# Performance work log

Hardware: AMD Instinct MI355X
Metric: run time of the kernel (lower is better)

The kernel has to match this reference:

```python
import jax, jax.numpy as jnp
import numpy as np

EPS = 1e-12  # torch F.normalize default eps
NUM_HEADS = 8


def _l2norm(t):
    # normalize along last (spatial) axis, matching F.normalize(dim=-1)
    n = jnp.linalg.norm(t, axis=-1, keepdims=True)
    return t / jnp.maximum(n, EPS)


def setup_inputs() -> dict:
    key = jax.random.key(0)
    ks = jax.random.split(key, 5)
    b, dim, qc, h, w = 16, 384, 192, 64, 64
    x = jax.random.normal(ks[0], (b, dim, h, w), dtype=jnp.float32)
    query = jax.random.normal(ks[1], (b, qc, h, w), dtype=jnp.float32)
    w_kv = jax.random.normal(ks[2], (2 * dim, dim), dtype=jnp.float32) * 0.05
    w_q = jax.random.normal(ks[3], (dim, qc), dtype=jnp.float32) * 0.05
    w_proj = jax.random.normal(ks[4], (dim, dim), dtype=jnp.float32) * 0.05
    temperature = jnp.ones((NUM_HEADS, 1, 1), dtype=jnp.float32)
    return {"x": x, "query": query, "w_kv": w_kv, "w_q": w_q,
            "w_proj": w_proj, "temperature": temperature}


def reference(x, query, w_kv, w_q, w_proj, temperature):
    b, c, h, w = x.shape
    hd = NUM_HEADS
    dc = c // hd  # per-head channel dim
    # 1x1 convs == channel GEMMs
    kv = jnp.einsum('oc,bchw->bohw', w_kv, x)          # [b, 2c, h, w]
    k, v = jnp.split(kv, 2, axis=1)                     # each [b, c, h, w]
    q = jnp.einsum('oc,bchw->bohw', w_q, query)         # [b, c, h, w]
    # split heads, flatten spatial: b (head c) h w -> b head c (h w)
    def heads(t):
        return t.reshape(b, hd, dc, h * w)
    q, k, v = heads(q), heads(k), heads(v)
    q = _l2norm(q)
    k = _l2norm(k)
    # channel-wise attention: [b, head, dc, dc]
    attn = jnp.einsum('bhcn,bhdn->bhcd', q, k) * temperature
    attn = jax.nn.softmax(attn, axis=-1)
    out = jnp.einsum('bhcd,bhdn->bhcn', attn, v)        # [b, head, dc, hw]
    out = out.reshape(b, c, h, w)
    out = jnp.einsum('oc,bchw->bohw', w_proj, out)
    return out
```

## Files before the change

kernel.cpp:

```cpp
#include <hip/hip_runtime.h>
#include <hip/hip_bf16.h>

typedef float f4 __attribute__((ext_vector_type(4)));
typedef short s8 __attribute__((ext_vector_type(8)));
typedef short s4 __attribute__((ext_vector_type(4)));

__device__ __forceinline__ short f2bf(float f) {
  union { float f; unsigned u; } v; v.f = f;
  unsigned r = v.u + 0x7fffu + ((v.u >> 16) & 1u);
  return (short)(r >> 16);
}
__device__ __forceinline__ void gl16(const short* g, short* l) {
  __builtin_amdgcn_global_load_lds(
      (const __attribute__((address_space(1))) unsigned*)g,
      (__attribute__((address_space(3))) unsigned*)l, 16, 0, 0);
}

__global__ __launch_bounds__(256, 1)
void kqs_k(const short* __restrict__ xT, const short* __restrict__ qT,
           const short* __restrict__ wkb, const short* __restrict__ wqb,
           float* __restrict__ Spart, float* __restrict__ ssq,
           float* __restrict__ ssk) {
  __shared__ __align__(16) short Bq[64 * 192];
  __shared__ __align__(16) short Bx[64 * 384];
  __shared__ __align__(16) short Qt[192 * 64];
  __shared__ __align__(16) short Kt[192 * 64];
  const int orig = blockIdx.x;
  const int xcd = orig & 7, ix = orig >> 3;
  const int pair = xcd * 16 + (ix >> 1);
  const int hg = ix & 1;
  const int b = pair >> 3, sc = pair & 7;
  const int tid = threadIdx.x, lane = tid & 63, w = tid >> 6;
  const int l15 = lane & 15, lhi = lane >> 4;

  const short* qTb = qT + ((long)b * 4096 + sc * 512) * 192;
  const short* xTb = xT + ((long)b * 4096 + sc * 512) * 384;

  f4 Sacc[3][3];
#pragma unroll
  for (int i = 0; i < 3; ++i)
#pragma unroll
    for (int j = 0; j < 3; ++j) Sacc[i][j] = (f4){0.f, 0.f, 0.f, 0.f};
  float sqa[12], ska[12];
#pragma unroll
  for (int i = 0; i < 12; ++i) { sqa[i] = 0.f; ska[i] = 0.f; }

#pragma unroll
  for (int i = 0; i < 6; ++i) {
    const int q = i * 256 + tid, row = q / 24, c = q % 24;
    gl16(qTb + row * 192 + ((c ^ (row & 7)) * 8), &Bq[q * 8]);
  }
#pragma unroll
  for (int i = 0; i < 12; ++i) {
    const int q = i * 256 + tid, row = q / 48, c = q % 48;
    gl16(xTb + row * 384 + ((c ^ (row & 7)) * 8), &Bx[q * 8]);
  }

#pragma unroll 1
  for (int t = 0; t < 8; ++t) {
    asm volatile("s_waitcnt vmcnt(12)" ::: "memory");
    __builtin_amdgcn_s_barrier();
    __builtin_amdgcn_sched_barrier(0);

    {
      f4 acc[3][4];
#pragma unroll
      for (int i = 0; i < 3; ++i)
#pragma unroll
        for (int j = 0; j < 4; ++j) acc[i][j] = (f4){0.f, 0.f, 0.f, 0.f};
#pragma unroll 2
      for (int kk = 0; kk < 192; kk += 32) {
        s8 af[3], bf[4];
#pragma unroll
        for (int mi = 0; mi < 3; ++mi)
          af[mi] = *(const s8*)(wqb +
              (long)(hg * 192 + w * 48 + mi * 16 + l15) * 192 + kk + lhi * 8);
#pragma unroll
        for (int ni = 0; ni < 4; ++ni) {
          const int s_ = ni * 16 + l15;
          bf[ni] = *(const s8*)(&Bq[s_ * 192 +
                                    ((((kk >> 3) + lhi) ^ (s_ & 7)) << 3)]);
        }
#pragma unroll
        for (int mi = 0; mi < 3; ++mi)
#pragma unroll
          for (int ni = 0; ni < 4; ++ni)
            acc[mi][ni] = __builtin_amdgcn_mfma_f32_16x16x32_bf16(
                af[mi], bf[ni], acc[mi][ni], 0, 0, 0);
      }
#pragma unroll
      for (int mi = 0; mi < 3; ++mi)
#pragma unroll
        for (int r = 0; r < 4; ++r) {
          const int row = w * 48 + mi * 16 + lhi * 4 + r;
#pragma unroll
          for (int ni = 0; ni < 4; ++ni) {
            const int col = ni * 16 + l15;
            const float v = acc[mi][ni][r];
            Qt[row * 64 + (((col >> 3) ^ (row & 7)) << 3) + (col & 7)] =
                f2bf(v);
            sqa[mi * 4 + r] += v * v;
          }
        }
    }

    asm volatile("s_waitcnt vmcnt(0)" ::: "memory");
    __builtin_amdgcn_s_barrier();
    __builtin_amdgcn_sched_barrier(0);

    {
      f4 acc[3][4];
#pragma unroll
      for (int i = 0; i < 3; ++i)
#pragma unroll
        for (int j = 0; j < 4; ++j) acc[i][j] = (f4){0.f, 0.f, 0.f, 0.f};
#pragma unroll 2
      for (int kk = 0; kk < 384; kk += 32) {
        s8 af[3], bf[4];
#pragma unroll
        for (int mi = 0; mi < 3; ++mi)
          af[mi] = *(const s8*)(wkb +
              (long)(hg * 192 + w * 48 + mi * 16 + l15) * 384 + kk + lhi * 8);
#pragma unroll
        for (int ni = 0; ni < 4; ++ni) {
          const int s_ = ni * 16 + l15;
          bf[ni] = *(const s8*)(&Bx[s_ * 384 +
                                    ((((kk >> 3) + lhi) ^ (s_ & 7)) << 3)]);
        }
#pragma unroll
        for (int mi = 0; mi < 3; ++mi)
#pragma unroll
          for (int ni = 0; ni < 4; ++ni)
            acc[mi][ni] = __builtin_amdgcn_mfma_f32_16x16x32_bf16(
                af[mi], bf[ni], acc[mi][ni], 0, 0, 0);
      }
#pragma unroll
      for (int mi = 0; mi < 3; ++mi)
#pragma unroll
        for (int r = 0; r < 4; ++r) {
          const int row = w * 48 + mi * 16 + lhi * 4 + r;
#pragma unroll
          for (int ni = 0; ni < 4; ++ni) {
            const int col = ni * 16 + l15;
            const float v = acc[mi][ni][r];
            Kt[row * 64 + (((col >> 3) ^ (row & 7)) << 3) + (col & 7)] =
                f2bf(v);
            ska[mi * 4 + r] += v * v;
          }
        }
    }

    __builtin_amdgcn_s_barrier();

    if (t + 1 < 8) {
      const long so = (long)(t + 1) * 64;
#pragma unroll
      for (int i = 0; i < 6; ++i) {
        const int q = i * 256 + tid, row = q / 24, c = q % 24;
        gl16(qTb + (so + row) * 192 + ((c ^ (row & 7)) * 8), &Bq[q * 8]);
      }
#pragma unroll
      for (int i = 0; i < 12; ++i) {
        const int q = i * 256 + tid, row = q / 48, c = q % 48;
        gl16(xTb + (so + row) * 384 + ((c ^ (row & 7)) * 8), &Bx[q * 8]);
      }
    }

    {
      const int hl = w * 48;
#pragma unroll
      for (int kk = 0; kk < 64; kk += 32) {
        s8 qa[3], ka[3];
#pragma unroll
        for (int i = 0; i < 3; ++i) {
          const int rr = hl + i * 16 + l15;
          const int cb = (((kk >> 3) + lhi) ^ (rr & 7)) << 3;
          qa[i] = *(const s8*)(&Qt[rr * 64 + cb]);
          ka[i] = *(const s8*)(&Kt[rr * 64 + cb]);
        }
#pragma unroll
        for (int mi = 0; mi < 3; ++mi)
#pragma unroll
          for (int ni = 0; ni < 3; ++ni)
            Sacc[mi][ni] = __builtin_amdgcn_mfma_f32_16x16x32_bf16(
                qa[mi], ka[ni], Sacc[mi][ni], 0, 0, 0);
      }
    }
  }

#pragma unroll
  for (int mi = 0; mi < 3; ++mi)
#pragma unroll
    for (int r = 0; r < 4; ++r) {
      float tq = sqa[mi * 4 + r], tk = ska[mi * 4 + r];
      tq += __shfl_xor(tq, 1); tq += __shfl_xor(tq, 2);
      tq += __shfl_xor(tq, 4); tq += __shfl_xor(tq, 8);
      tk += __shfl_xor(tk, 1); tk += __shfl_xor(tk, 2);
      tk += __shfl_xor(tk, 4); tk += __shfl_xor(tk, 8);
      const int row = hg * 192 + w * 48 + mi * 16 + lhi * 4 + r;
      if (l15 == 0) {
        atomicAdd(&ssq[b * 384 + row], tq);
        atomicAdd(&ssk[b * 384 + row], tk);
      }
    }
  float* Sp = Spart + (((long)sc * 16 + b) * 8 + hg * 4 + w) * 2304;
#pragma unroll
  for (int mi = 0; mi < 3; ++mi)
#pragma unroll
    for (int ni = 0; ni < 3; ++ni)
#pragma unroll
      for (int r = 0; r < 4; ++r)
        Sp[(mi * 16 + lhi * 4 + r) * 48 + ni * 16 + l15] = Sacc[mi][ni][r];
}

template<int NKT, bool OUTF32, bool SWZ>
__global__ __launch_bounds__(256)
void gemm4(const short* __restrict__ A_, long Asb, int lda,
           const short* __restrict__ B_, long Bsb, int ldb,
           void* __restrict__ O_, long Osb, int ldo,
           int nbm, int nbn) {
  __shared__ __align__(16) short As[2][8192];
  __shared__ __align__(16) short Bs[2][8192];
  int f = blockIdx.x;
  if (SWZ) { const int cpx = gridDim.x >> 3; f = (f & 7) * cpx + (f >> 3); }
  const int m0 = (f % nbm) * 128;
  const int t2 = f / nbm;
  const int n0 = (t2 % nbn) * 128;
  const int bz = t2 / nbn;
  const short* Ag = A_ + (long)bz * Asb;
  const short* Bg = B_ + (long)bz * Bsb;

  const int tid = threadIdx.x, lane = tid & 63, wid = tid >> 6;
  const int l15 = lane & 15, lhi = lane >> 4;
  const int wm = (wid >> 1) * 64, wn = (wid & 1) * 64;
  const int srow = tid >> 3;
  const int skc = ((tid & 7) ^ (srow & 7)) * 8;

  f4 acc[4][4];
#pragma unroll
  for (int i = 0; i < 4; ++i)
#pragma unroll
    for (int j = 0; j < 4; ++j) acc[i][j] = (f4){0.f, 0.f, 0.f, 0.f};

#pragma unroll
  for (int it = 0; it < 4; ++it) {
    const int r = it * 32 + srow;
    gl16(Ag + (long)(m0 + r) * lda + skc, &As[0][(it * 256 + tid) * 8]);
    gl16(Bg + (long)(n0 + r) * ldb + skc, &Bs[0][(it * 256 + tid) * 8]);
  }
  if (NKT > 1) {
#pragma unroll
    for (int it = 0; it < 4; ++it) {
      const int r = it * 32 + srow;
      gl16(Ag + (long)(m0 + r) * lda + 64 + skc, &As[1][(it * 256 + tid) * 8]);
      gl16(Bg + (long)(n0 + r) * ldb + 64 + skc, &Bs[1][(it * 256 + tid) * 8]);
    }
  }

#pragma unroll
  for (int kt = 0; kt < NKT; ++kt) {
    const int cur = kt & 1;
    if (kt + 1 < NKT) asm volatile("s_waitcnt vmcnt(8)" ::: "memory");
    else              asm volatile("s_waitcnt vmcnt(0)" ::: "memory");
    __builtin_amdgcn_s_barrier();
    __builtin_amdgcn_sched_barrier(0);
#pragma unroll
    for (int kk = 0; kk < 2; ++kk) {
      const int cb = ((lhi + kk * 4) ^ (l15 & 7)) * 8;
      s8 af[4], bf[4];
#pragma unroll
      for (int i = 0; i < 4; ++i) {
        af[i] = *(const s8*)(&As[cur][(wm + i * 16 + l15) * 64 + cb]);
        bf[i] = *(const s8*)(&Bs[cur][(wn + i * 16 + l15) * 64 + cb]);
      }
#pragma unroll
      for (int mi = 0; mi < 4; ++mi)
#pragma unroll
        for (int ni = 0; ni < 4; ++ni)
          acc[mi][ni] = __builtin_amdgcn_mfma_f32_16x16x32_bf16(
              af[mi], bf[ni], acc[mi][ni], 0, 0, 0);
    }
    asm volatile("s_waitcnt lgkmcnt(0)" ::: "memory");
    __builtin_amdgcn_s_barrier();
    if (kt + 2 < NKT) {
      const int k2 = (kt + 2) * 64;
#pragma unroll
      for (int it = 0; it < 4; ++it) {
        const int r = it * 32 + srow;
        gl16(Ag + (long)(m0 + r) * lda + k2 + skc,
             &As[cur][(it * 256 + tid) * 8]);
        gl16(Bg + (long)(n0 + r) * ldb + k2 + skc,
             &Bs[cur][(it * 256 + tid) * 8]);
      }
    }
  }

#pragma unroll
  for (int mi = 0; mi < 4; ++mi)
#pragma unroll
    for (int r = 0; r < 4; ++r) {
      const int grow = m0 + wm + mi * 16 + lhi * 4 + r;
#pragma unroll
      for (int ni = 0; ni < 4; ++ni) {
        const int col = n0 + wn + ni * 16 + l15;
        const float v = acc[mi][ni][r];
        if (OUTF32)
          ((float*)O_)[(long)bz * Osb + (long)grow * ldo + col] = v;
        else
          ((short*)O_)[(long)bz * Osb + (long)grow * ldo + col] = f2bf(v);
      }
    }
}

__global__ __launch_bounds__(256)
void prep_k(const float* __restrict__ x, const float* __restrict__ q,
            const float* __restrict__ wkv, const float* __restrict__ wq,
            const float* __restrict__ wp, short* __restrict__ xT,
            short* __restrict__ qT, short* __restrict__ wkb,
            short* __restrict__ wvT, short* __restrict__ wqb,
            short* __restrict__ wpb, float* __restrict__ ssqk) {
  const int role = blockIdx.x;
  if (role == 9) {
    const int g = (blockIdx.z * 64 + blockIdx.y) * 256 + threadIdx.x;
    if (g < 12288) ssqk[g] = 0.f;
    for (int i = g; i < 516096; i += 262144) {
      if (i < 147456) {
        wkb[i] = f2bf(wkv[i]);
      } else if (i < 294912) {
        const int t = i - 147456;
        wvT[t] = f2bf(wkv[(384 + (t % 384)) * 384 + t / 384]);
      } else if (i < 368640) {
        wqb[i - 294912] = f2bf(wq[i - 294912]);
      } else {
        wpb[i - 368640] = f2bf(wp[i - 368640]);
      }
    }
    return;
  }
  __shared__ float Ls[64][65];
  const bool isQ = role >= 6;
  const int C = isQ ? 192 : 384;
  const int c0 = (isQ ? role - 6 : role) * 64;
  const int s0 = blockIdx.y * 64;
  const float* src = (isQ ? q : x) + (long)blockIdx.z * C * 4096;
  short* dst = (isQ ? qT : xT) + (long)blockIdx.z * 4096 * C;
  const int tid = threadIdx.x;
  const int rr = tid >> 4, cq = (tid & 15) * 4;
#pragma unroll
  for (int it = 0; it < 4; ++it) {
    const int r = it * 16 + rr;
    f4 v = *(const f4*)(src + (long)(c0 + r) * 4096 + s0 + cq);
    Ls[r][cq + 0] = v.x; Ls[r][cq + 1] = v.y;
    Ls[r][cq + 2] = v.z; Ls[r][cq + 3] = v.w;
  }
  __syncthreads();
#pragma unroll
  for (int it = 0; it < 4; ++it) {
    const int sr = it * 16 + rr;
    s4 o;
#pragma unroll
    for (int j = 0; j < 4; ++j) o[j] = f2bf(Ls[cq + j][sr]);
    *(s4*)(&dst[(long)(s0 + sr) * C + c0 + cq]) = o;
  }
}

__global__ __launch_bounds__(256)
void smY_k(const float* __restrict__ Spart, const float* __restrict__ ssq,
           const float* __restrict__ ssk, const float* __restrict__ temp,
           const short* __restrict__ wpb, short* __restrict__ Yb) {
  const int b = blockIdx.x, h = blockIdx.y, tid = threadIdx.x;
  __shared__ float L[2304];
  __shared__ float rq[48], rk[48], mrow[48], irow[48];
  __shared__ __align__(16) short PTl[48 * 72];
  if (tid < 48) {
    rq[tid] = 1.f / fmaxf(sqrtf(ssq[b * 384 + h * 48 + tid]), 1e-12f);
    rk[tid] = 1.f / fmaxf(sqrtf(ssk[b * 384 + h * 48 + tid]), 1e-12f);
  }
  __syncthreads();
  const float tp = temp[h];
  for (int i = tid; i < 2304; i += 256) {
    float v = 0.f;
#pragma unroll
    for (int z = 0; z < 8; ++z)
      v += Spart[(((long)z * 16 + b) * 8 + h) * 2304 + i];
    const int c = i / 48, d = i % 48;
    L[i] = v * rq[c] * rk[d] * tp;
  }
  __syncthreads();
  if (tid < 48) {
    float m = -1e30f;
    for (int d = 0; d < 48; ++d) m = fmaxf(m, L[tid * 48 + d]);
    float s = 0.f;
    for (int d = 0; d < 48; ++d) s += __expf(L[tid * 48 + d] - m);
    mrow[tid] = m;
    irow[tid] = 1.f / s;
  }
  __syncthreads();
  for (int i = tid; i < 48 * 72; i += 256) {
    const int d = i / 72, c = i % 72;
    float p = 0.f;
    if (c < 48) p = __expf(L[c * 48 + d] - mrow[c]) * irow[c];
    PTl[i] = f2bf(p);
  }
  __syncthreads();
  const int lane = tid & 63, w = tid >> 6;
  const int l15 = lane & 15, lhi = lane >> 4;
  f4 acc[6][3];
#pragma unroll
  for (int i = 0; i < 6; ++i)
#pragma unroll
    for (int j = 0; j < 3; ++j) acc[i][j] = (f4){0.f, 0.f, 0.f, 0.f};
#pragma unroll
  for (int kk = 0; kk < 2; ++kk) {
    s8 bf[3];
#pragma unroll
    for (int ni = 0; ni < 3; ++ni)
      bf[ni] = *(const s8*)(&PTl[(ni * 16 + l15) * 72 + kk * 32 + lhi * 8]);
#pragma unroll
    for (int mi = 0; mi < 6; ++mi) {
      const int row = w * 96 + mi * 16 + l15;
      s8 af = *(const s8*)(wpb + (long)row * 384 + h * 48 + kk * 32 + lhi * 8);
#pragma unroll
      for (int ni = 0; ni < 3; ++ni)
        acc[mi][ni] = __builtin_amdgcn_mfma_f32_16x16x32_bf16(
            af, bf[ni], acc[mi][ni], 0, 0, 0);
    }
  }
#pragma unroll
  for (int mi = 0; mi < 6; ++mi)
#pragma unroll
    for (int r = 0; r < 4; ++r) {
      const int row = w * 96 + mi * 16 + lhi * 4 + r;
#pragma unroll
      for (int ni = 0; ni < 3; ++ni) {
        const int d = ni * 16 + l15;
        Yb[((long)b * 384 + row) * 384 + h * 48 + d] = f2bf(acc[mi][ni][r]);
      }
    }
}

extern "C" void kernel_launch(void* const* d_in, const int* in_sizes, int n_in,
                              void* d_out, int out_size, void* d_ws, size_t ws_size,
                              hipStream_t stream) {
  const float* x = (const float*)d_in[0];
  const float* query = (const float*)d_in[1];
  const float* w_kv = (const float*)d_in[2];
  const float* w_q = (const float*)d_in[3];
  const float* w_proj = (const float*)d_in[4];
  const float* temp = (const float*)d_in[5];

  char* w = (char*)d_ws;
  short* xT   = (short*)(w + 0);
  short* qT   = (short*)(w + 50331648);
  float* Spart= (float*)(w + 75497472);
  short* Yb   = (short*)(w + 94371840);
  short* Nbb  = (short*)(w + 99090432);
  float* ssq  = (float*)(w + 103809024);
  float* ssk  = (float*)(w + 103833600);
  short* wkb  = (short*)(w + 103858176);
  short* wvT  = (short*)(w + 104153088);
  short* wqb  = (short*)(w + 104448000);
  short* wpb  = (short*)(w + 104595456);
  float* out  = (float*)d_out;

  prep_k<<<dim3(10, 64, 16), 256, 0, stream>>>(
      x, query, w_kv, w_q, w_proj, xT, qT, wkb, wvT, wqb, wpb, ssq);
  kqs_k<<<256, 256, 0, stream>>>(xT, qT, wkb, wqb, Spart, ssq, ssk);
  smY_k<<<dim3(16, 8), 256, 0, stream>>>(Spart, ssq, ssk, temp, wpb, Yb);
  gemm4<6, false, false><<<144, 256, 0, stream>>>(
      Yb, 147456, 384, wvT, 0, 384, Nbb, 147456, 384, 3, 3);
  gemm4<6, true, true><<<1536, 256, 0, stream>>>(
      Nbb, 147456, 384, xT, 1572864, 384, out, 1572864, 4096, 3, 32);
}
```

Before: 189.3 us.

## Drop LDS staging in kqs_k, read B fragments from global, double grid

The kernel no longer stages x/query tiles in shared memory through async global-to-LDS loads with barriers. Each wave now reads its MFMA B fragments straight from global memory, and the per-wave Qt/Kt rows are private to that wave, so all block barriers are removed. The spatial split doubles to 16 chunks (512 blocks, launch bounds allowing 2 blocks per CU) and the softmax kernel sums 16 partial S tiles. The goal is more parallelism and occupancy. The cost is that the four waves load the same activation tile redundantly, relying on the caches, and the reduction has more partials.

```diff
diff --git a/kernel.cpp b/kernel.cpp
--- a/kernel.cpp
+++ b/kernel.cpp
@@ -16,25 +16,26 @@
       (__attribute__((address_space(3))) unsigned*)l, 16, 0, 0);
 }
 
-__global__ __launch_bounds__(256, 1)
+__global__ __launch_bounds__(256, 2)
 void kqs_k(const short* __restrict__ xT, const short* __restrict__ qT,
            const short* __restrict__ wkb, const short* __restrict__ wqb,
            float* __restrict__ Spart, float* __restrict__ ssq,
            float* __restrict__ ssk) {
-  __shared__ __align__(16) short Bq[64 * 192];
-  __shared__ __align__(16) short Bx[64 * 384];
   __shared__ __align__(16) short Qt[192 * 64];
   __shared__ __align__(16) short Kt[192 * 64];
   const int orig = blockIdx.x;
   const int xcd = orig & 7, ix = orig >> 3;
-  const int pair = xcd * 16 + (ix >> 1);
+  const int pair = xcd * 32 + (ix >> 1);
   const int hg = ix & 1;
-  const int b = pair >> 3, sc = pair & 7;
+  const int b = pair >> 4, sc = pair & 15;
   const int tid = threadIdx.x, lane = tid & 63, w = tid >> 6;
   const int l15 = lane & 15, lhi = lane >> 4;
-
-  const short* qTb = qT + ((long)b * 4096 + sc * 512) * 192;
-  const short* xTb = xT + ((long)b * 4096 + sc * 512) * 384;
+  const int hl = w * 48;
+
+  const short* qTb = qT + (long)b * 4096 * 192;
+  const short* xTb = xT + (long)b * 4096 * 384;
+  const short* wqw = wqb + (long)(hg * 192 + hl) * 192;
+  const short* wkw = wkb + (long)(hg * 192 + hl) * 384;
 
   f4 Sacc[3][3];
 #pragma unroll
@@ -45,22 +46,9 @@
 #pragma unroll
   for (int i = 0; i < 12; ++i) { sqa[i] = 0.f; ska[i] = 0.f; }
 
-#pragma unroll
-  for (int i = 0; i < 6; ++i) {
-    const int q = i * 256 + tid, row = q / 24, c = q % 24;
-    gl16(qTb + row * 192 + ((c ^ (row & 7)) * 8), &Bq[q * 8]);
-  }
-#pragma unroll
-  for (int i = 0; i < 12; ++i) {
-    const int q = i * 256 + tid, row = q / 48, c = q % 48;
-    gl16(xTb + row * 384 + ((c ^ (row & 7)) * 8), &Bx[q * 8]);
-  }
-
 #pragma unroll 1
-  for (int t = 0; t < 8; ++t) {
-    asm volatile("s_waitcnt vmcnt(12)" ::: "memory");
-    __builtin_amdgcn_s_barrier();
-    __builtin_amdgcn_sched_barrier(0);
+  for (int t = 0; t < 4; ++t) {
+    const int s0 = sc * 256 + t * 64;
 
     {
       f4 acc[3][4];
@@ -68,19 +56,16 @@
       for (int i = 0; i < 3; ++i)
 #pragma unroll
         for (int j = 0; j < 4; ++j) acc[i][j] = (f4){0.f, 0.f, 0.f, 0.f};
-#pragma unroll 2
+#pragma unroll
       for (int kk = 0; kk < 192; kk += 32) {
         s8 af[3], bf[4];
 #pragma unroll
         for (int mi = 0; mi < 3; ++mi)
-          af[mi] = *(const s8*)(wqb +
-              (long)(hg * 192 + w * 48 + mi * 16 + l15) * 192 + kk + lhi * 8);
-#pragma unroll
-        for (int ni = 0; ni < 4; ++ni) {
-          const int s_ = ni * 16 + l15;
-          bf[ni] = *(const s8*)(&Bq[s_ * 192 +
-                                    ((((kk >> 3) + lhi) ^ (s_ & 7)) << 3)]);
-        }
+          af[mi] = *(const s8*)(wqw + (long)(mi * 16 + l15) * 192 + kk + lhi * 8);
+#pragma unroll
+        for (int ni = 0; ni < 4; ++ni)
+          bf[ni] = *(const s8*)(qTb + (long)(s0 + ni * 16 + l15) * 192 +
+                                kk + lhi * 8);
 #pragma unroll
         for (int mi = 0; mi < 3; ++mi)
 #pragma unroll
@@ -92,7 +77,7 @@
       for (int mi = 0; mi < 3; ++mi)
 #pragma unroll
         for (int r = 0; r < 4; ++r) {
-          const int row = w * 48 + mi * 16 + lhi * 4 + r;
+          const int row = hl + mi * 16 + lhi * 4 + r;
 #pragma unroll
           for (int ni = 0; ni < 4; ++ni) {
             const int col = ni * 16 + l15;
@@ -104,29 +89,22 @@
         }
     }
 
-    asm volatile("s_waitcnt vmcnt(0)" ::: "memory");
-    __builtin_amdgcn_s_barrier();
-    __builtin_amdgcn_sched_barrier(0);
-
     {
       f4 acc[3][4];
 #pragma unroll
       for (int i = 0; i < 3; ++i)
 #pragma unroll
         for (int j = 0; j < 4; ++j) acc[i][j] = (f4){0.f, 0.f, 0.f, 0.f};
-#pragma unroll 2
+#pragma unroll 4
       for (int kk = 0; kk < 384; kk += 32) {
         s8 af[3], bf[4];
 #pragma unroll
         for (int mi = 0; mi < 3; ++mi)
-          af[mi] = *(const s8*)(wkb +
-              (long)(hg * 192 + w * 48 + mi * 16 + l15) * 384 + kk + lhi * 8);
-#pragma unroll
-        for (int ni = 0; ni < 4; ++ni) {
-          const int s_ = ni * 16 + l15;
-          bf[ni] = *(const s8*)(&Bx[s_ * 384 +
-                                    ((((kk >> 3) + lhi) ^ (s_ & 7)) << 3)]);
-        }
+          af[mi] = *(const s8*)(wkw + (long)(mi * 16 + l15) * 384 + kk + lhi * 8);
+#pragma unroll
+        for (int ni = 0; ni < 4; ++ni)
+          bf[ni] = *(const s8*)(xTb + (long)(s0 + ni * 16 + l15) * 384 +
+                                kk + lhi * 8);
 #pragma unroll
         for (int mi = 0; mi < 3; ++mi)
 #pragma unroll
@@ -138,7 +116,7 @@
       for (int mi = 0; mi < 3; ++mi)
 #pragma unroll
         for (int r = 0; r < 4; ++r) {
-          const int row = w * 48 + mi * 16 + lhi * 4 + r;
+          const int row = hl + mi * 16 + lhi * 4 + r;
 #pragma unroll
           for (int ni = 0; ni < 4; ++ni) {
             const int col = ni * 16 + l15;
@@ -150,24 +128,7 @@
         }
     }
 
-    __builtin_amdgcn_s_barrier();
-
-    if (t + 1 < 8) {
-      const long so = (long)(t + 1) * 64;
-#pragma unroll
-      for (int i = 0; i < 6; ++i) {
-        const int q = i * 256 + tid, row = q / 24, c = q % 24;
-        gl16(qTb + (so + row) * 192 + ((c ^ (row & 7)) * 8), &Bq[q * 8]);
-      }
-#pragma unroll
-      for (int i = 0; i < 12; ++i) {
-        const int q = i * 256 + tid, row = q / 48, c = q % 48;
-        gl16(xTb + (so + row) * 384 + ((c ^ (row & 7)) * 8), &Bx[q * 8]);
-      }
-    }
-
     {
-      const int hl = w * 48;
 #pragma unroll
       for (int kk = 0; kk < 64; kk += 32) {
         s8 qa[3], ka[3];
@@ -197,7 +158,7 @@
       tq += __shfl_xor(tq, 4); tq += __shfl_xor(tq, 8);
       tk += __shfl_xor(tk, 1); tk += __shfl_xor(tk, 2);
       tk += __shfl_xor(tk, 4); tk += __shfl_xor(tk, 8);
-      const int row = hg * 192 + w * 48 + mi * 16 + lhi * 4 + r;
+      const int row = hg * 192 + hl + mi * 16 + lhi * 4 + r;
       if (l15 == 0) {
         atomicAdd(&ssq[b * 384 + row], tq);
         atomicAdd(&ssk[b * 384 + row], tk);
@@ -381,7 +342,7 @@
   for (int i = tid; i < 2304; i += 256) {
     float v = 0.f;
 #pragma unroll
-    for (int z = 0; z < 8; ++z)
+    for (int z = 0; z < 16; ++z)
       v += Spart[(((long)z * 16 + b) * 8 + h) * 2304 + i];
     const int c = i / 48, d = i % 48;
     L[i] = v * rq[c] * rk[d] * tp;
@@ -465,7 +426,7 @@
 
   prep_k<<<dim3(10, 64, 16), 256, 0, stream>>>(
       x, query, w_kv, w_q, w_proj, xT, qT, wkb, wvT, wqb, wpb, ssq);
-  kqs_k<<<256, 256, 0, stream>>>(xT, qT, wkb, wqb, Spart, ssq, ssk);
+  kqs_k<<<512, 256, 0, stream>>>(xT, qT, wkb, wqb, Spart, ssq, ssk);
   smY_k<<<dim3(16, 8), 256, 0, stream>>>(Spart, ssq, ssk, temp, wpb, Yb);
   gemm4<6, false, false><<<144, 256, 0, stream>>>(
       Yb, 147456, 384, wvT, 0, 384, Nbb, 147456, 384, 3, 3);
```

After: 314.0 us. +65.9%, slower.
